# Performance work log

Measured on AMD Instinct MI355X. Metric: run time of the kernel, lower is better.

The kernel has to match this reference:

```python
import jax, jax.numpy as jnp
import numpy as np
from functools import partial

NUM_CLASSES = 80
INPUT_SIZE = 416
ANCHORS_NP = np.array([[10,13],[16,30],[33,23],[30,61],[62,45],[59,119],[116,90],[156,198],[373,326]], dtype=np.float32)
LAMBDA_OBJ, LAMBDA_NOOBJ, LAMBDA_COORD, LAMBDA_CLASS = 5.0, 1.0, 1.0, 1.0
IGNORE_THR = 0.5


def _encode_one(target_b, layer_idx, layer_h, layer_w):
    # target_b: [T,5]; sequential scan reproduces torch's overwrite-in-order semantics
    A, C = 3, NUM_CLASSES
    anchors = jnp.asarray(ANCHORS_NP)              # [9,2] in input pixels
    la = anchors[3*layer_idx:3*layer_idx+3]        # this layer's anchors
    scaled_aw = la[:, 0] * (layer_w / INPUT_SIZE)
    scaled_ah = la[:, 1] * (layer_h / INPUT_SIZE)

    init = (jnp.zeros((A, layer_h, layer_w)),      # mask
            jnp.ones((A, layer_h, layer_w)),       # noobj_mask
            jnp.zeros((A, layer_h, layer_w)),      # tx
            jnp.zeros((A, layer_h, layer_w)),      # ty
            jnp.zeros((A, layer_h, layer_w)),      # tw
            jnp.zeros((A, layer_h, layer_w)),      # th
            jnp.zeros((A, layer_h, layer_w)),      # tconf
            jnp.zeros((A, layer_h, layer_w, C)))   # tcls

    def step(carry, ann):
        mask, noobj, tx, ty, tw, th, tconf, tcls = carry
        valid = ann.sum() > 0
        # IoU of gt box vs all 9 anchors, both anchored at origin
        gw_px = ann[2] * INPUT_SIZE
        gh_px = ann[3] * INPUT_SIZE
        inter = jnp.minimum(gw_px, anchors[:, 0]) * jnp.minimum(gh_px, anchors[:, 1])
        union = gw_px * gh_px + anchors[:, 0] * anchors[:, 1] - inter
        iou = inter / (union + 1e-16)               # [9]
        best_n = jnp.argmax(iou)
        in_layer = (best_n >= 3*layer_idx) & (best_n < 3*layer_idx + 3)
        do = valid & in_layer
        bl = jnp.clip(best_n - 3*layer_idx, 0, 2)   # local best anchor
        gx = ann[0] * layer_w
        gy = ann[1] * layer_h
        gw_g = ann[2] * layer_w
        gh_g = ann[3] * layer_h
        gi = jnp.clip(gx.astype(jnp.int32), 0, layer_w - 1)
        gj = jnp.clip(gy.astype(jnp.int32), 0, layer_h - 1)
        iou_local = iou[3*layer_idx:3*layer_idx + 3]
        noobj_upd = noobj.at[:, gj, gi].set(jnp.where(iou_local > IGNORE_THR, 0.0, noobj[:, gj, gi]))
        noobj = jnp.where(do, noobj_upd, noobj)
        upd = lambda arr, val: jnp.where(do, arr.at[bl, gj, gi].set(val), arr)
        mask = upd(mask, 1.0)
        tx = upd(tx, gx - gi)
        ty = upd(ty, gy - gj)
        tw = upd(tw, gw_g / scaled_aw[bl])
        th = upd(th, gh_g / scaled_ah[bl])
        tconf = upd(tconf, 1.0)
        cid = jnp.clip(ann[4].astype(jnp.int32), 0, C - 1)
        tcls = jnp.where(do, tcls.at[bl, gj, gi, cid].set(1.0), tcls)
        return (mask, noobj, tx, ty, tw, th, tconf, tcls), None

    out, _ = jax.lax.scan(step, init, target_b)
    return out


def encode_layer(target, layer_idx, layer_h, layer_w):
    return jax.vmap(lambda tb: _encode_one(tb, layer_idx, layer_h, layer_w))(target)


def layer_loss(pred, target, layer_idx):
    B, _, H, W = pred.shape
    C = NUM_CLASSES
    p = pred.reshape(B, 3, 5 + C, H, W).transpose(0, 1, 3, 4, 2)  # [B,3,H,W,5+C]
    px = jax.nn.sigmoid(p[..., 0])
    py = jax.nn.sigmoid(p[..., 1])
    pw = jnp.exp(p[..., 2])
    ph = jnp.exp(p[..., 3])
    pconf = jax.nn.sigmoid(p[..., 4])
    pcls = jax.nn.sigmoid(p[..., 5:])
    mask, noobj, tx, ty, tw, th, tconf, tcls = encode_layer(target, layer_idx, H, W)
    sq = lambda a, b: jnp.sum((a - b) ** 2)
    box = LAMBDA_COORD * (sq(px*mask, tx) + sq(py*mask, ty) + sq(pw*mask, tw) + sq(ph*mask, th))
    obj = LAMBDA_OBJ * sq(pconf * mask, tconf)
    no_obj = LAMBDA_NOOBJ * jnp.sum((pconf * noobj) ** 2)
    # masked BCE-sum == sum over all cells of bce * mask (tcls is 0 off-mask)
    logp = jnp.maximum(jnp.log(pcls), -100.0)
    log1mp = jnp.maximum(jnp.log1p(-pcls), -100.0)
    bce = -(tcls * logp + (1.0 - tcls) * log1mp)
    cls = LAMBDA_CLASS * jnp.sum(bce * mask[..., None])
    return box + obj + no_obj + cls


def setup_inputs() -> dict:
    key = jax.random.key(0)
    ks = jax.random.split(key, 6)
    B, T = 32, 50
    p3 = jax.random.normal(ks[0], (B, 255, 52, 52), dtype=jnp.float32)
    p4 = jax.random.normal(ks[1], (B, 255, 26, 26), dtype=jnp.float32)
    p5 = jax.random.normal(ks[2], (B, 255, 13, 13), dtype=jnp.float32)
    cxcy = jax.random.uniform(ks[3], (B, T, 2), minval=0.02, maxval=0.98)
    wh = jax.random.uniform(ks[4], (B, T, 2), minval=0.02, maxval=0.4)
    cid = jax.random.randint(ks[5], (B, T, 1), 0, NUM_CLASSES).astype(jnp.float32)
    target = jnp.concatenate([cxcy, wh, cid], axis=-1)
    return {"p3": p3, "p4": p4, "p5": p5, "target": target}


def reference(p3, p4, p5, target):
    B = p3.shape[0]
    loss = 0.0
    for layer_idx, pred in enumerate([p3, p4, p5]):
        loss = loss + layer_loss(pred, target, layer_idx)
    return loss / B
```

## Files before the change

### kernel.cpp

```cpp
#include <hip/hip_runtime.h>
#include <math.h>

#define NUM_CLASSES 80
#define T_ANN 50
#define IGNORE_THR 0.5f
#define NCONF_BLOCKS 512
#define NENC_BLOCKS 96

__device__ __constant__ float ANCHORS[9][2] = {
    {10.f,13.f},{16.f,30.f},{33.f,23.f},{30.f,61.f},{62.f,45.f},
    {59.f,119.f},{116.f,90.f},{156.f,198.f},{373.f,326.f}};

__device__ inline float sigmoidf_(float x) { return 1.f / (1.f + __expf(-x)); }

__device__ inline float block_reduce_sum(float v) {
    for (int o = 32; o > 0; o >>= 1) v += __shfl_down(v, o, 64);
    __shared__ float smem[4];
    int lane = threadIdx.x & 63, w = threadIdx.x >> 6;
    if (lane == 0) smem[w] = v;
    __syncthreads();
    float s = 0.f;
    if (threadIdx.x == 0) {
        int nw = (blockDim.x + 63) >> 6;
        for (int i = 0; i < nw; i++) s += smem[i];
    }
    return s;
}

template <int HW>
__device__ inline float conf_seg(const float* __restrict__ P, int B,
                                 int gtid, int nthr) {
    float acc = 0.f;
    const int total = B * 3 * HW;
    for (int e = gtid; e < total; e += nthr) {
        int plane = e / HW;
        int pix = e - plane * HW;
        int b = plane / 3;
        int a = plane - 3 * b;
        float x = P[((size_t)(b * 255 + a * 85 + 4)) * HW + pix];
        float s = sigmoidf_(x);
        acc += s * s;
    }
    return acc;
}

__global__ __launch_bounds__(256) void k_conf(
    const float* __restrict__ p3, const float* __restrict__ p4,
    const float* __restrict__ p5, float* __restrict__ ws, int B) {
    int gtid = blockIdx.x * blockDim.x + threadIdx.x;
    int nthr = gridDim.x * blockDim.x;
    float acc = conf_seg<52 * 52>(p3, B, gtid, nthr) +
                conf_seg<26 * 26>(p4, B, gtid, nthr) +
                conf_seg<13 * 13>(p5, B, gtid, nthr);
    float bs = block_reduce_sum(acc);
    if (threadIdx.x == 0) ws[blockIdx.x] = bs;
}

__global__ __launch_bounds__(256) void k_encode(
    const float* __restrict__ p3, const float* __restrict__ p4,
    const float* __restrict__ p5, const float* __restrict__ target,
    float* __restrict__ ws) {
    const int b = blockIdx.x / 3;
    const int L = blockIdx.x % 3;
    const int W = (L == 0) ? 52 : (L == 1) ? 26 : 13;
    const int H = W, HW = H * W;
    const float* P = (L == 0) ? p3 : (L == 1) ? p4 : p5;

    __shared__ int s_key[T_ANN];
    __shared__ int s_cell[T_ANN];
    __shared__ int s_bl[T_ANN], s_ign[T_ANN], s_cid[T_ANN], s_final[T_ANN];
    __shared__ float s_tx[T_ANN], s_ty[T_ANN], s_tw[T_ANN], s_th[T_ANN];
    __shared__ unsigned s_cls[T_ANN][3];
    __shared__ int s_iok[3 * T_ANN];
    __shared__ int s_ilist[3 * T_ANN];
    __shared__ int s_flist[T_ANN];
    __shared__ int s_wcnt[4], s_woff[4], s_nf, s_ni;

    const int tid = threadIdx.x;
    const int lane = tid & 63, wv = tid >> 6;

    if (tid < 3 * T_ANN) s_iok[tid] = 1;
    if (tid < T_ANN) {
        const float* ann = target + ((size_t)b * T_ANN + tid) * 5;
        float a0 = ann[0], a1 = ann[1], a2 = ann[2], a3 = ann[3], a4 = ann[4];
        bool valid = (a0 + a1 + a2 + a3 + a4) > 0.f;
        float gwpx = a2 * 416.f, ghpx = a3 * 416.f;
        float best = -1.f; int bestn = 0;
        float iouL[3];
        for (int k = 0; k < 9; k++) {
            float aw = ANCHORS[k][0], ah = ANCHORS[k][1];
            float inter = fminf(gwpx, aw) * fminf(ghpx, ah);
            float uni = gwpx * ghpx + aw * ah - inter;
            float iou = inter / (uni + 1e-16f);
            if (iou > best) { best = iou; bestn = k; }
            if (k >= 3 * L && k < 3 * L + 3) iouL[k - 3 * L] = iou;
        }
        bool inlayer = (bestn >= 3 * L) && (bestn < 3 * L + 3);
        bool dof = valid && inlayer;
        int ign = 0;
        for (int a = 0; a < 3; a++) if (iouL[a] > IGNORE_THR) ign |= (1 << a);

        int key = -1, cell = -1, bl = 0;
        float tx = 0.f, ty = 0.f, tw = 0.f, th = 0.f;
        if (dof) {
            bl = bestn - 3 * L;
            float gx = a0 * W, gy = a1 * H;
            int gi = min(W - 1, max(0, (int)gx));
            int gj = min(H - 1, max(0, (int)gy));
            cell = gj * W + gi;
            key = (bl << 12) | cell;
            float saw = ANCHORS[3 * L + bl][0] * ((float)W / 416.f);
            float sah = ANCHORS[3 * L + bl][1] * ((float)H / 416.f);
            tx = gx - (float)gi; ty = gy - (float)gj;
            tw = (a2 * W) / saw;  th = (a3 * H) / sah;
        }
        int cid = (int)a4; cid = max(0, min(NUM_CLASSES - 1, cid));
        s_key[tid] = key; s_cell[tid] = cell; s_bl[tid] = bl;
        s_ign[tid] = ign; s_cid[tid] = cid;
        s_tx[tid] = tx; s_ty[tid] = ty; s_tw[tid] = tw; s_th[tid] = th;
        s_final[tid] = (key >= 0);
        s_cls[tid][0] = 0u; s_cls[tid][1] = 0u; s_cls[tid][2] = 0u;
    }
    __syncthreads();

    for (int idx = tid; idx < T_ANN * T_ANN; idx += 256) {
        int t = idx / T_ANN, t2 = idx - t * T_ANN;
        if (t2 > t && s_key[t] >= 0 && s_key[t] == s_key[t2]) s_final[t] = 0;
    }
    for (int idx = tid; idx < 3 * T_ANN * T_ANN; idx += 256) {
        int e = idx / T_ANN, t2 = idx - e * T_ANN;
        int t = e / 3, a = e - 3 * t;
        if (t2 < t && s_cell[t] >= 0 && ((s_ign[t] >> a) & 1) &&
            s_cell[t2] == s_cell[t] && ((s_ign[t2] >> a) & 1))
            s_iok[e] = 0;
    }
    __syncthreads();

    for (int idx = tid; idx < T_ANN * T_ANN; idx += 256) {
        int t = idx / T_ANN, t2 = idx - t * T_ANN;
        if (s_final[t] && s_key[t2] == s_key[t]) {
            int c = s_cid[t2];
            atomicOr(&s_cls[t][c >> 5], 1u << (c & 31));
        }
    }
    if (wv == 0) {
        bool p = (tid < T_ANN) && s_final[tid];
        unsigned long long m = __ballot(p);
        if (p) s_flist[__popcll(m & ((1ull << lane) - 1ull))] = tid;
        if (lane == 0) s_nf = __popcll(m);
    }
    {
        bool ok = false; int pack = 0;
        if (tid < 3 * T_ANN) {
            int t = tid / 3, a = tid - 3 * t;
            ok = s_iok[tid] && (s_cell[t] >= 0) && ((s_ign[t] >> a) & 1);
            pack = (a << 12) | (s_cell[t] & 4095);
        }
        unsigned long long m = __ballot(ok);
        if (lane == 0) s_wcnt[wv] = __popcll(m);
        __syncthreads();
        if (tid == 0) {
            int off = 0;
            for (int w = 0; w < 4; w++) { s_woff[w] = off; off += s_wcnt[w]; }
            s_ni = off;
        }
        __syncthreads();
        if (ok) s_ilist[s_woff[wv] + __popcll(m & ((1ull << lane) - 1ull))] = pack;
    }
    __syncthreads();

    float corr = 0.f;
    const int nf = s_nf, ni = s_ni;

    for (int idx = tid; idx < nf * 85; idx += 256) {
        int f = idx / 85, r = idx - f * 85;
        int t = s_flist[f];
        int bl = s_bl[t], cell = s_cell[t];
        float x = P[((size_t)(b * 255 + bl * 85 + r)) * HW + cell];
        if (r < 2) {
            float d = sigmoidf_(x) - (r == 0 ? s_tx[t] : s_ty[t]);
            corr += d * d;
        } else if (r < 4) {
            float d = __expf(x) - (r == 2 ? s_tw[t] : s_th[t]);
            corr += d * d;
        } else if (r == 4) {
            float d = sigmoidf_(x) - 1.f;
            corr += 5.f * d * d;
        } else {
            int c = r - 5;
            unsigned bit = (s_cls[t][c >> 5] >> (c & 31)) & 1u;
            float ax = fabsf(x);
            float l = __logf(1.f + __expf(-ax));
            float ls_pos = (x >= 0.f) ? -l : x - l;
            float ls_neg = (x >= 0.f) ? -x - l : -l;
            float logp   = fmaxf(ls_pos, -100.f);
            float log1mp = fmaxf(ls_neg, -100.f);
            corr += bit ? -logp : -log1mp;
        }
    }
    for (int idx = tid; idx < ni; idx += 256) {
        int pack = s_ilist[idx];
        int a = pack >> 12, cell = pack & 4095;
        float s = sigmoidf_(P[((size_t)(b * 255 + a * 85 + 4)) * HW + cell]);
        corr -= s * s;
    }

    float bs = block_reduce_sum(corr);
    if (tid == 0) ws[NCONF_BLOCKS + blockIdx.x] = bs;
}

__global__ __launch_bounds__(256) void k_final(
    const float* __restrict__ ws, float* __restrict__ out, int n, float invB) {
    float a = 0.f;
    for (int i = threadIdx.x; i < n; i += 256) a += ws[i];
    float s = block_reduce_sum(a);
    if (threadIdx.x == 0) out[0] = s * invB;
}

extern "C" void kernel_launch(void* const* d_in, const int* in_sizes, int n_in,
                              void* d_out, int out_size, void* d_ws, size_t ws_size,
                              hipStream_t stream) {
    const float* p3 = (const float*)d_in[0];
    const float* p4 = (const float*)d_in[1];
    const float* p5 = (const float*)d_in[2];
    const float* tg = (const float*)d_in[3];
    float* out = (float*)d_out;
    float* ws = (float*)d_ws;

    const int B = in_sizes[3] / (T_ANN * 5);

    k_conf<<<NCONF_BLOCKS, 256, 0, stream>>>(p3, p4, p5, ws, B);
    k_encode<<<B * 3, 256, 0, stream>>>(p3, p4, p5, tg, ws);
    k_final<<<1, 256, 0, stream>>>(ws, out, NCONF_BLOCKS + B * 3, 1.f / (float)B);
}
```

Measured before the change: 150.5 us.

## Merge conf-reduction and encode kernels into one launch with float4 loads

```diff
diff --git a/kernel.cpp b/kernel.cpp
--- a/kernel.cpp
+++ b/kernel.cpp
@@ -4,8 +4,7 @@
 #define NUM_CLASSES 80
 #define T_ANN 50
 #define IGNORE_THR 0.5f
-#define NCONF_BLOCKS 512
-#define NENC_BLOCKS 96
+#define NCONF_BLOCKS 384
 
 __device__ __constant__ float ANCHORS[9][2] = {
     {10.f,13.f},{16.f,30.f},{33.f,23.f},{30.f,61.f},{62.f,45.f},
@@ -21,47 +20,61 @@
     __syncthreads();
     float s = 0.f;
     if (threadIdx.x == 0) {
-        int nw = (blockDim.x + 63) >> 6;
-        for (int i = 0; i < nw; i++) s += smem[i];
+        for (int i = 0; i < 4; i++) s += smem[i];
     }
     return s;
 }
 
-template <int HW>
-__device__ inline float conf_seg(const float* __restrict__ P, int B,
-                                 int gtid, int nthr) {
-    float acc = 0.f;
-    const int total = B * 3 * HW;
-    for (int e = gtid; e < total; e += nthr) {
-        int plane = e / HW;
-        int pix = e - plane * HW;
-        int b = plane / 3;
-        int a = plane - 3 * b;
-        float x = P[((size_t)(b * 255 + a * 85 + 4)) * HW + pix];
-        float s = sigmoidf_(x);
-        acc += s * s;
-    }
-    return acc;
-}
-
-__global__ __launch_bounds__(256) void k_conf(
-    const float* __restrict__ p3, const float* __restrict__ p4,
-    const float* __restrict__ p5, float* __restrict__ ws, int B) {
-    int gtid = blockIdx.x * blockDim.x + threadIdx.x;
-    int nthr = gridDim.x * blockDim.x;
-    float acc = conf_seg<52 * 52>(p3, B, gtid, nthr) +
-                conf_seg<26 * 26>(p4, B, gtid, nthr) +
-                conf_seg<13 * 13>(p5, B, gtid, nthr);
-    float bs = block_reduce_sum(acc);
-    if (threadIdx.x == 0) ws[blockIdx.x] = bs;
-}
-
-__global__ __launch_bounds__(256) void k_encode(
+__global__ __launch_bounds__(256) void k_main(
     const float* __restrict__ p3, const float* __restrict__ p4,
     const float* __restrict__ p5, const float* __restrict__ target,
-    float* __restrict__ ws) {
-    const int b = blockIdx.x / 3;
-    const int L = blockIdx.x % 3;
+    float* __restrict__ ws, int B) {
+    const int tid = threadIdx.x;
+
+    if ((int)blockIdx.x < NCONF_BLOCKS) {
+        const int n1 = B * 3 * 676;
+        const int n2 = B * 3 * 169;
+        const int n3 = B * 3 * 169;
+        const int total = n1 + n2 + n3;
+        float acc = 0.f;
+        for (int idx = blockIdx.x * 256 + tid; idx < total;
+             idx += NCONF_BLOCKS * 256) {
+            if (idx < n1) {
+                int plane = idx / 676, r = idx - plane * 676;
+                int b = plane / 3, a = plane - 3 * b;
+                const float4* p =
+                    (const float4*)(p3 + (size_t)(b * 255 + a * 85 + 4) * 2704) + r;
+                float4 v = *p;
+                float s0 = sigmoidf_(v.x), s1 = sigmoidf_(v.y);
+                float s2 = sigmoidf_(v.z), s3 = sigmoidf_(v.w);
+                acc += s0 * s0 + s1 * s1 + s2 * s2 + s3 * s3;
+            } else if (idx < n1 + n2) {
+                int e = idx - n1;
+                int plane = e / 169, r = e - plane * 169;
+                int b = plane / 3, a = plane - 3 * b;
+                const float4* p =
+                    (const float4*)(p4 + (size_t)(b * 255 + a * 85 + 4) * 676) + r;
+                float4 v = *p;
+                float s0 = sigmoidf_(v.x), s1 = sigmoidf_(v.y);
+                float s2 = sigmoidf_(v.z), s3 = sigmoidf_(v.w);
+                acc += s0 * s0 + s1 * s1 + s2 * s2 + s3 * s3;
+            } else {
+                int e = idx - n1 - n2;
+                int plane = e / 169, pix = e - plane * 169;
+                int b = plane / 3, a = plane - 3 * b;
+                float x = p5[(size_t)(b * 255 + a * 85 + 4) * 169 + pix];
+                float s = sigmoidf_(x);
+                acc += s * s;
+            }
+        }
+        float bs = block_reduce_sum(acc);
+        if (tid == 0) ws[blockIdx.x] = bs;
+        return;
+    }
+
+    const int bid = (int)blockIdx.x - NCONF_BLOCKS;
+    const int b = bid / 3;
+    const int L = bid % 3;
     const int W = (L == 0) ? 52 : (L == 1) ? 26 : 13;
     const int H = W, HW = H * W;
     const float* P = (L == 0) ? p3 : (L == 1) ? p4 : p5;
@@ -76,7 +89,6 @@
     __shared__ int s_flist[T_ANN];
     __shared__ int s_wcnt[4], s_woff[4], s_nf, s_ni;
 
-    const int tid = threadIdx.x;
     const int lane = tid & 63, wv = tid >> 6;
 
     if (tid < 3 * T_ANN) s_iok[tid] = 1;
@@ -206,7 +218,7 @@
     }
 
     float bs = block_reduce_sum(corr);
-    if (tid == 0) ws[NCONF_BLOCKS + blockIdx.x] = bs;
+    if (tid == 0) ws[blockIdx.x] = bs;
 }
 
 __global__ __launch_bounds__(256) void k_final(
@@ -228,8 +240,8 @@
     float* ws = (float*)d_ws;
 
     const int B = in_sizes[3] / (T_ANN * 5);
-
-    k_conf<<<NCONF_BLOCKS, 256, 0, stream>>>(p3, p4, p5, ws, B);
-    k_encode<<<B * 3, 256, 0, stream>>>(p3, p4, p5, tg, ws);
-    k_final<<<1, 256, 0, stream>>>(ws, out, NCONF_BLOCKS + B * 3, 1.f / (float)B);
-}
+    const int nblocks = NCONF_BLOCKS + 3 * B;
+
+    k_main<<<nblocks, 256, 0, stream>>>(p3, p4, p5, tg, ws, B);
+    k_final<<<1, 256, 0, stream>>>(ws, out, nblocks, 1.f / (float)B);
+}
```

After: 145.3 us. -3.4%, faster.
